# Kernel tuning notes

Measured on AMD Instinct MI355X. Metric: run time of the kernel, lower is better.

The kernel has to match this reference:

```python
import jax, jax.numpy as jnp
import numpy as np

H = 256   # hidden_dim
S = 16    # d_state
B = 2
N = 8192
LN_EPS = 1e-5


def setup_inputs() -> dict:
    key = jax.random.key(0)
    ks = jax.random.split(key, 12)
    std = 1.0 / np.sqrt(H)
    inp = {
        'x': jax.random.normal(ks[0], (B, N, H), dtype=jnp.float32),
        'in_w': jax.random.normal(ks[1], (2 * H, H), dtype=jnp.float32) * std,
        'in_b': jax.random.normal(ks[2], (2 * H,), dtype=jnp.float32) * std,
        'xp_w': jax.random.normal(ks[3], (2 * S + 1, H), dtype=jnp.float32) * std,
        'xp_b': jax.random.normal(ks[4], (2 * S + 1,), dtype=jnp.float32) * std,
        'dt_w': jax.random.normal(ks[5], (H, 1), dtype=jnp.float32),
        'dt_b': jax.random.normal(ks[6], (H,), dtype=jnp.float32),
        'A_log': jnp.log(jnp.broadcast_to(jnp.arange(1, S + 1, dtype=jnp.float32), (H, S))),
        'D': jnp.ones((H,), dtype=jnp.float32),
        'out_w': jax.random.normal(ks[7], (H, H), dtype=jnp.float32) * std,
        'out_b': jax.random.normal(ks[8], (H,), dtype=jnp.float32) * std,
        'ln_g': jnp.ones((H,), dtype=jnp.float32),
        'ln_b': jnp.zeros((H,), dtype=jnp.float32),
    }
    return inp


def reference(x, in_w, in_b, xp_w, xp_b, dt_w, dt_b, A_log, D, out_w, out_b, ln_g, ln_b):
    # x: (B, N, H). Dropout is identity in eval mode.
    residual = x
    xz = jnp.einsum('bnh,kh->bnk', x, in_w) + in_b            # (B,N,2H)
    x_inner, z = xz[..., :H], xz[..., H:]
    x_dbl = jnp.einsum('bnh,kh->bnk', x_inner, xp_w) + xp_b   # (B,N,2S+1)
    dt_raw = x_dbl[..., :1]
    B_raw = x_dbl[..., 1:S + 1]                               # (B,N,S)
    C_raw = x_dbl[..., S + 1:]                                # (B,N,S)
    dt = jax.nn.softplus(dt_raw * dt_w[:, 0] + dt_b)          # (B,N,H)
    # NOTE: the original computes dA = exp(dt * A) but never uses it; A_log
    # does not affect the output, so we skip materializing dA.
    dB = dt[..., None] * B_raw[:, :, None, :]                 # (B,N,H,S)
    h = jnp.cumsum(x_inner[..., None] * dB, axis=1)           # (B,N,H,S)
    y = jnp.einsum('bnhs,bns->bnh', h, C_raw) + D * x_inner   # (B,N,H)
    y = y * jax.nn.silu(z)
    out = jnp.einsum('bnh,kh->bnk', y, out_w) + out_b
    r = out + residual
    mu = jnp.mean(r, axis=-1, keepdims=True)
    var = jnp.mean((r - mu) ** 2, axis=-1, keepdims=True)
    return ln_g * (r - mu) * jax.lax.rsqrt(var + LN_EPS) + ln_b
```

## Files before the change

kernel.cpp:

```cpp
#include <hip/hip_runtime.h>
#include <hip/hip_bf16.h>


#define HD 256
#define SD 16
#define NSEQ 8192
#define NBATCH 2
#define BN (NBATCH * NSEQ)
#define CHUNK 32
#define NCHUNK (NSEQ / CHUNK)
#define NGRP 16
#define GSZ (NCHUNK / NGRP)
#define LN_EPS 1e-5f

#define NX  (BN * HD)
#define NIW (2 * HD * HD)
#define NXP (48 * HD)
#define NOW (HD * HD)

typedef __hip_bfloat16 bf16;
typedef __attribute__((ext_vector_type(8))) short bf16x8;
typedef __attribute__((ext_vector_type(4))) short short4v;
typedef __attribute__((ext_vector_type(4))) float f32x4;

__device__ __forceinline__ float b2f(bf16 v) { return __bfloat162float(v); }
__device__ __forceinline__ short f2bs(float f) {
  union { bf16 b; short s; } u;
  u.b = __float2bfloat16(f);
  return u.s;
}
__device__ __forceinline__ bf16x8 cvt_frag(const float* p) {
  bf16x8 r;
#pragma unroll
  for (int j = 0; j < 8; ++j) r[j] = f2bs(p[j]);
  return r;
}
__device__ __forceinline__ float softplus_f(float a) {
  return (a > 20.f) ? a : __logf(1.f + __expf(a));
}

__global__ __launch_bounds__(256) void k0_convert(
    const float* __restrict__ x, const float* __restrict__ in_w,
    const float* __restrict__ xp_w, const float* __restrict__ out_w,
    bf16* __restrict__ xb, bf16* __restrict__ wbin,
    bf16* __restrict__ wbxp, bf16* __restrict__ wbout)
{
  const int base = (blockIdx.x * 256 + threadIdx.x) * 4;
  if (base < NX) {
    f32x4 v = *(const f32x4*)(x + base);
    *(short4v*)((short*)xb + base) =
        short4v{f2bs(v[0]), f2bs(v[1]), f2bs(v[2]), f2bs(v[3])};
  } else if (base < NX + NIW) {
    const int off = base - NX;
    f32x4 v = *(const f32x4*)(in_w + off);
    *(short4v*)((short*)wbin + off) =
        short4v{f2bs(v[0]), f2bs(v[1]), f2bs(v[2]), f2bs(v[3])};
  } else if (base < NX + NIW + NXP) {
    const int off = base - NX - NIW;
    short4v s;
    if (off < 33 * HD) {
      f32x4 v = *(const f32x4*)(xp_w + off);
      s = short4v{f2bs(v[0]), f2bs(v[1]), f2bs(v[2]), f2bs(v[3])};
    } else {
      s = short4v{0, 0, 0, 0};
    }
    *(short4v*)((short*)wbxp + off) = s;
  } else if (base < NX + NIW + NXP + NOW) {
    const int off = base - NX - NIW - NXP;
    f32x4 v = *(const f32x4*)(out_w + off);
    *(short4v*)((short*)wbout + off) =
        short4v{f2bs(v[0]), f2bs(v[1]), f2bs(v[2]), f2bs(v[3])};
  }
}

__global__ __launch_bounds__(256) void k1_gemm(
    const bf16* __restrict__ xb, const bf16* __restrict__ wbin,
    const float* __restrict__ in_b, bf16* __restrict__ xib,
    bf16* __restrict__ zb)
{
  __shared__ __align__(16) char smem[128 * 264 * 2];
  bf16* Bt = (bf16*)smem;
  float* Ct = (float*)smem;

  const int tid = threadIdx.x;
  const int rt = blockIdx.x >> 2, ct = blockIdx.x & 3;
  const int R0 = rt * 128, C0 = ct * 128;
  const int wave = tid >> 6, lane = tid & 63, q = lane >> 4, l16 = lane & 15;

#pragma unroll
  for (int it = 0; it < 16; ++it) {
    const int f = tid + it * 256;
    const int row = f >> 5, g = f & 31;
    bf16x8 v = *(const bf16x8*)(wbin + (size_t)(C0 + row) * HD + g * 8);
    *(bf16x8*)(Bt + row * 264 + g * 8) = v;
  }
  __syncthreads();

  const int rowHalf = (wave & 1) * 64;
  const int colHalf = (wave >> 1) * 64;
  f32x4 acc[4][4] = {};
  const bf16* ap = xb + (size_t)(R0 + rowHalf + l16) * HD + q * 8;
#pragma unroll
  for (int k = 0; k < HD; k += 32) {
    bf16x8 a[4], b[4];
#pragma unroll
    for (int i = 0; i < 4; ++i)
      a[i] = *(const bf16x8*)(ap + (size_t)i * 16 * HD + k);
#pragma unroll
    for (int j = 0; j < 4; ++j)
      b[j] = *(const bf16x8*)(Bt + (colHalf + j * 16 + l16) * 264 + k + q * 8);
#pragma unroll
    for (int i = 0; i < 4; ++i)
#pragma unroll
      for (int j = 0; j < 4; ++j)
        acc[i][j] = __builtin_amdgcn_mfma_f32_16x16x32_bf16(a[i], b[j], acc[i][j], 0, 0, 0);
  }
  __syncthreads();

#pragma unroll
  for (int j = 0; j < 4; ++j) {
    const int col = colHalf + j * 16 + l16;
    const float bias = in_b[C0 + col];
#pragma unroll
    for (int i = 0; i < 4; ++i)
#pragma unroll
      for (int r = 0; r < 4; ++r)
        Ct[(rowHalf + i * 16 + q * 4 + r) * 132 + col] = acc[i][j][r] + bias;
  }
  __syncthreads();

  bf16* dst = (C0 < HD) ? xib : zb;
  const int Cd = (C0 < HD) ? C0 : (C0 - HD);
#pragma unroll
  for (int it = 0; it < 8; ++it) {
    const int f = tid + it * 256;
    const int row = f >> 4, g = f & 15;
    bf16x8 v = cvt_frag(Ct + row * 132 + g * 8);
    *(bf16x8*)(dst + (size_t)(R0 + row) * HD + Cd + g * 8) = v;
  }
}

__global__ __launch_bounds__(256) void k2_xp_sum(
    const bf16* __restrict__ xib, const bf16* __restrict__ wbxp,
    const float* __restrict__ xp_b, const float* __restrict__ dt_w,
    const float* __restrict__ dt_b, float* __restrict__ dbc,
    float* __restrict__ Mc)
{
  __shared__ bf16 xt[32 * 264];
  __shared__ bf16 wp[48 * 264];
  __shared__ float sdbc[32][33];
  const int tid = threadIdx.x;
  const int R0 = blockIdx.x * CHUNK;
  const int wave = tid >> 6, lane = tid & 63, q = lane >> 4, l16 = lane & 15;

#pragma unroll
  for (int it = 0; it < 4; ++it) {
    const int f = tid + it * 256, row = f >> 5, g = f & 31;
    *(bf16x8*)(xt + row * 264 + g * 8) =
        *(const bf16x8*)(xib + (size_t)(R0 + row) * HD + g * 8);
  }
#pragma unroll
  for (int it = 0; it < 6; ++it) {
    const int f = tid + it * 256, row = f >> 5, g = f & 31;
    *(bf16x8*)(wp + row * 264 + g * 8) =
        *(const bf16x8*)(wbxp + (size_t)row * HD + g * 8);
  }
  __syncthreads();

  if (wave < 2) {
    f32x4 pacc[3] = {};
#pragma unroll
    for (int k = 0; k < HD; k += 32) {
      bf16x8 af = *(const bf16x8*)(xt + (wave * 16 + l16) * 264 + k + q * 8);
#pragma unroll
      for (int t = 0; t < 3; ++t) {
        bf16x8 bfr = *(const bf16x8*)(wp + (t * 16 + l16) * 264 + k + q * 8);
        pacc[t] = __builtin_amdgcn_mfma_f32_16x16x32_bf16(af, bfr, pacc[t], 0, 0, 0);
      }
    }
#pragma unroll
    for (int t = 0; t < 3; ++t) {
      const int col = t * 16 + l16;
      if (col < 33) {
        const float bias = xp_b[col];
#pragma unroll
        for (int r = 0; r < 4; ++r)
          sdbc[wave * 16 + q * 4 + r][col] = pacc[t][r] + bias;
      }
    }
  }
  __syncthreads();

  {
    const float* sflat = &sdbc[0][0];
    for (int idx = tid; idx < CHUNK * 33; idx += 256)
      dbc[(size_t)R0 * 33 + idx] = sflat[idx];
  }
  {
    const int h = tid;
    const float dtw = dt_w[h], dtb = dt_b[h];
    float st[SD] = {};
#pragma unroll
    for (int n = 0; n < CHUNK; ++n) {
      const float xv = b2f(xt[n * 264 + h]);
      const float dt = softplus_f(sdbc[n][0] * dtw + dtb);
      const float u = xv * dt;
#pragma unroll
      for (int s = 0; s < SD; ++s) st[s] += u * sdbc[n][1 + s];
    }
    const int b = R0 >> 13, c = (R0 & (NSEQ - 1)) >> 5;
    float* mp = Mc + ((size_t)(b * NCHUNK + c)) * 4096 + h;
#pragma unroll
    for (int s = 0; s < SD; ++s) mp[s * HD] = st[s];
  }
}

__global__ __launch_bounds__(256) void k4a_prefix_local(
    float* __restrict__ Mc, float* __restrict__ Gs)
{
  const int tid = blockIdx.x * 256 + threadIdx.x;
  const int b = tid >> 16;
  const int g = (tid >> 12) & (NGRP - 1);
  const int hs = tid & 4095;
  float run = 0.f;
#pragma unroll
  for (int i = 0; i < GSZ; ++i) {
    const size_t idx = ((size_t)(b * NCHUNK + g * GSZ + i)) * 4096 + hs;
    const float v = Mc[idx];
    Mc[idx] = run;
    run += v;
  }
  Gs[((size_t)(b * NGRP + g)) * 4096 + hs] = run;
}

__global__ __launch_bounds__(256) void k4b_prefix_groups(float* __restrict__ Gs)
{
  const int tid = blockIdx.x * 256 + threadIdx.x;
  const int b = tid >> 12;
  const int hs = tid & 4095;
  float run = 0.f;
#pragma unroll
  for (int g = 0; g < NGRP; ++g) {
    const size_t idx = ((size_t)(b * NGRP + g)) * 4096 + hs;
    const float v = Gs[idx];
    Gs[idx] = run;
    run += v;
  }
}

__global__ __launch_bounds__(512) void k56_scan_out_ln(
    const bf16* __restrict__ xib, const bf16* __restrict__ zb,
    const float* __restrict__ dbc, const float* __restrict__ dt_w,
    const float* __restrict__ dt_b, const float* __restrict__ Dv,
    const float* __restrict__ Mc, const float* __restrict__ Gs,
    const bf16* __restrict__ wbout, const float* __restrict__ out_b,
    const float* __restrict__ x, const float* __restrict__ ln_g,
    const float* __restrict__ ln_b, float* __restrict__ out)
{
  __shared__ float sdbc[CHUNK][33];
  __shared__ float yt[32][260];
  __shared__ float pt[32][260];
  const int tid = threadIdx.x;
  const int wave = tid >> 6, lane = tid & 63, q = lane >> 4, l16 = lane & 15;
  const int R0 = blockIdx.x * CHUNK;
  const int b = R0 >> 13;
  const int cchunk = (R0 & (NSEQ - 1)) >> 5;

  for (int idx = tid; idx < CHUNK * 33; idx += 512) {
    const int n = idx / 33, j = idx - n * 33;
    sdbc[n][j] = dbc[(size_t)(R0 + n) * 33 + j];
  }
  __syncthreads();

  {
    const int h = tid & 255;
    const int sh = tid >> 8;
    const float dtw = dt_w[h], dtb = dt_b[h];
    const float dv = Dv[h];
    float st[8];
    const float* mp = Mc + ((size_t)(b * NCHUNK + cchunk)) * 4096 + sh * 8 * HD + h;
    const float* gp = Gs + ((size_t)(b * NGRP + cchunk / GSZ)) * 4096 + sh * 8 * HD + h;
#pragma unroll
    for (int s = 0; s < 8; ++s) st[s] = mp[s * HD] + gp[s * HD];
    float (*dst)[260] = (sh == 0) ? yt : pt;
    for (int n = 0; n < CHUNK; ++n) {
      const float xv = b2f(xib[(size_t)(R0 + n) * HD + h]);
      const float dt = softplus_f(sdbc[n][0] * dtw + dtb);
      const float u = xv * dt;
      float y = (sh == 0) ? dv * xv : 0.f;
#pragma unroll
      for (int s = 0; s < 8; ++s) {
        st[s] += u * sdbc[n][1 + sh * 8 + s];
        y += st[s] * sdbc[n][17 + sh * 8 + s];
      }
      dst[n][h] = y;
    }
  }
  __syncthreads();

  {
    const int h = tid & 255;
    const int r2 = tid >> 8;
#pragma unroll
    for (int j = 0; j < 16; ++j) {
      const int row = r2 * 16 + j;
      const float zv = b2f(zb[(size_t)(R0 + row) * HD + h]);
      const float sig = 1.f / (1.f + __expf(-zv));
      yt[row][h] = (yt[row][h] + pt[row][h]) * zv * sig;
    }
  }
  __syncthreads();

  const int cw = wave * 32;
  f32x4 acc[2][2] = {};
#pragma unroll
  for (int k = 0; k < HD; k += 32) {
    bf16x8 a0 = cvt_frag(&yt[l16][k + q * 8]);
    bf16x8 a1 = cvt_frag(&yt[16 + l16][k + q * 8]);
#pragma unroll
    for (int t = 0; t < 2; ++t) {
      bf16x8 bfr = *(const bf16x8*)(wbout + (size_t)(cw + t * 16 + l16) * HD + k + q * 8);
      acc[0][t] = __builtin_amdgcn_mfma_f32_16x16x32_bf16(a0, bfr, acc[0][t], 0, 0, 0);
      acc[1][t] = __builtin_amdgcn_mfma_f32_16x16x32_bf16(a1, bfr, acc[1][t], 0, 0, 0);
    }
  }
  __syncthreads();

#pragma unroll
  for (int t = 0; t < 2; ++t) {
    const int col = cw + t * 16 + l16;
    const float bias = out_b[col];
#pragma unroll
    for (int i = 0; i < 2; ++i)
#pragma unroll
      for (int r = 0; r < 4; ++r) {
        const int row = i * 16 + q * 4 + r;
        pt[row][col] = acc[i][t][r] + bias + x[(size_t)(R0 + row) * HD + col];
      }
  }
  __syncthreads();

#pragma unroll
  for (int rr = 0; rr < 4; ++rr) {
    const int row = wave * 4 + rr;
    float p = 0.f;
#pragma unroll
    for (int j = 0; j < 4; ++j) p += pt[row][lane + 64 * j];
#pragma unroll
    for (int off = 32; off > 0; off >>= 1) p += __shfl_xor(p, off);
    const float mu = p * (1.f / 256.f);
    float v2 = 0.f;
#pragma unroll
    for (int j = 0; j < 4; ++j) {
      const float d = pt[row][lane + 64 * j] - mu;
      v2 += d * d;
    }
#pragma unroll
    for (int off = 32; off > 0; off >>= 1) v2 += __shfl_xor(v2, off);
    const float rstd = rsqrtf(v2 * (1.f / 256.f) + LN_EPS);
    const size_t base = (size_t)(R0 + row) * HD;
#pragma unroll
    for (int j = 0; j < 4; ++j) {
      const int cc = lane + 64 * j;
      out[base + cc] = ln_g[cc] * (pt[row][cc] - mu) * rstd + ln_b[cc];
    }
  }
}

extern "C" void kernel_launch(void* const* d_in, const int* in_sizes, int n_in,
                              void* d_out, int out_size, void* d_ws, size_t ws_size,
                              hipStream_t stream)
{
  const float* x     = (const float*)d_in[0];
  const float* in_w  = (const float*)d_in[1];
  const float* in_b  = (const float*)d_in[2];
  const float* xp_w  = (const float*)d_in[3];
  const float* xp_b  = (const float*)d_in[4];
  const float* dt_w  = (const float*)d_in[5];
  const float* dt_b  = (const float*)d_in[6];
  const float* Dv    = (const float*)d_in[8];
  const float* out_w = (const float*)d_in[9];
  const float* out_b = (const float*)d_in[10];
  const float* ln_g  = (const float*)d_in[11];
  const float* ln_b  = (const float*)d_in[12];

  char* ws = (char*)d_ws;
  bf16*  xib   = (bf16*)(ws);
  bf16*  zb    = (bf16*)(ws +  8388608);
  bf16*  xb    = (bf16*)(ws + 16777216);
  float* dbc   = (float*)(ws + 25165824);
  float* Mc    = (float*)(ws + 27328512);
  float* Gs    = (float*)(ws + 35717120);
  bf16*  wbin  = (bf16*)(ws + 36241408);
  bf16*  wbxp  = (bf16*)(ws + 36503552);
  bf16*  wbout = (bf16*)(ws + 36528128);
  float* out   = (float*)d_out;

  hipLaunchKernelGGL(k0_convert, dim3((NX + NIW + NXP + NOW) / 1024), dim3(256),
                     0, stream, x, in_w, xp_w, out_w, xb, wbin, wbxp, wbout);
  hipLaunchKernelGGL(k1_gemm, dim3(512), dim3(256), 0, stream,
                     xb, wbin, in_b, xib, zb);
  hipLaunchKernelGGL(k2_xp_sum, dim3(BN / CHUNK), dim3(256), 0, stream,
                     xib, wbxp, xp_b, dt_w, dt_b, dbc, Mc);
  hipLaunchKernelGGL(k4a_prefix_local, dim3(NBATCH * NGRP * 4096 / 256),
                     dim3(256), 0, stream, Mc, Gs);
  hipLaunchKernelGGL(k4b_prefix_groups, dim3(NBATCH * 4096 / 256), dim3(256),
                     0, stream, Gs);
  hipLaunchKernelGGL(k56_scan_out_ln, dim3(BN / CHUNK), dim3(512), 0, stream,
                     xib, zb, dbc, dt_w, dt_b, Dv, Mc, Gs,
                     wbout, out_b, x, ln_g, ln_b, out);
}
```

Measured before the change: 150.3 us.

## Reformulate chunked SSM scan as MFMA matmuls with precomputed masked C·B tile

The per-chunk state sums and the intra-chunk scan become bf16 MFMA products. The chunk-end state is B^T·U. The output is a causal-masked (C·B^T)·U plus C·H_prev, with the masked 32x32 T matrix computed in the xp kernel and passed through global memory. This replaces the serial per-thread scalar recurrence over 16 states and 32 timesteps with matrix-core work, and shrinks the output kernel to 256 threads with reused shared memory. In exchange, the scan state, B, C and u are rounded to bf16, which lowers accuracy, and an extra global buffer write and read is added.

```diff
diff --git a/kernel.cpp b/kernel.cpp
--- a/kernel.cpp
+++ b/kernel.cpp
@@ -12,6 +12,8 @@
 #define NGRP 16
 #define GSZ (NCHUNK / NGRP)
 #define LN_EPS 1e-5f
+#define UST 40
+#define YST 257
 
 #define NX  (BN * HD)
 #define NIW (2 * HD * HD)
@@ -22,12 +24,18 @@
 typedef __attribute__((ext_vector_type(8))) short bf16x8;
 typedef __attribute__((ext_vector_type(4))) short short4v;
 typedef __attribute__((ext_vector_type(4))) float f32x4;
+typedef __attribute__((ext_vector_type(4))) unsigned int uint4v;
+typedef __attribute__((ext_vector_type(2))) unsigned int uint2v;
 
 __device__ __forceinline__ float b2f(bf16 v) { return __bfloat162float(v); }
 __device__ __forceinline__ short f2bs(float f) {
   union { bf16 b; short s; } u;
   u.b = __float2bfloat16(f);
   return u.s;
+}
+__device__ __forceinline__ unsigned int pack2(float a, float b) {
+  return (unsigned int)(unsigned short)f2bs(a) |
+         ((unsigned int)(unsigned short)f2bs(b) << 16);
 }
 __device__ __forceinline__ bf16x8 cvt_frag(const float* p) {
   bf16x8 r;
@@ -140,18 +148,21 @@
   }
 }
 
-__global__ __launch_bounds__(256) void k2_xp_sum(
+__global__ __launch_bounds__(256) void kS_xp_sum(
     const bf16* __restrict__ xib, const bf16* __restrict__ wbxp,
     const float* __restrict__ xp_b, const float* __restrict__ dt_w,
     const float* __restrict__ dt_b, float* __restrict__ dbc,
-    float* __restrict__ Mc)
-{
-  __shared__ bf16 xt[32 * 264];
-  __shared__ bf16 wp[48 * 264];
-  __shared__ float sdbc[32][33];
+    bf16* __restrict__ Tg, float* __restrict__ Mc)
+{
+  __shared__ __align__(16) bf16 xt[32 * 264];
+  __shared__ __align__(16) bf16 wp[48 * 264];
+  __shared__ __align__(16) float sdbc[32][33];
+  __shared__ __align__(16) bf16 sBt[16 * UST];
+  __shared__ __align__(16) bf16 Ut[256 * UST];
   const int tid = threadIdx.x;
-  const int R0 = blockIdx.x * CHUNK;
   const int wave = tid >> 6, lane = tid & 63, q = lane >> 4, l16 = lane & 15;
+  const int cix = blockIdx.x;
+  const int R0 = cix * CHUNK;
 
 #pragma unroll
   for (int it = 0; it < 4; ++it) {
@@ -184,8 +195,13 @@
       if (col < 33) {
         const float bias = xp_b[col];
 #pragma unroll
-        for (int r = 0; r < 4; ++r)
-          sdbc[wave * 16 + q * 4 + r][col] = pacc[t][r] + bias;
+        for (int r = 0; r < 4; ++r) {
+          const int row = wave * 16 + q * 4 + r;
+          const float v = pacc[t][r] + bias;
+          sdbc[row][col] = v;
+          if (col >= 1 && col < 17)
+            *((short*)sBt + (col - 1) * UST + row) = f2bs(v);
+        }
       }
     }
   }
@@ -199,19 +215,57 @@
   {
     const int h = tid;
     const float dtw = dt_w[h], dtb = dt_b[h];
-    float st[SD] = {};
-#pragma unroll
-    for (int n = 0; n < CHUNK; ++n) {
-      const float xv = b2f(xt[n * 264 + h]);
-      const float dt = softplus_f(sdbc[n][0] * dtw + dtb);
-      const float u = xv * dt;
-#pragma unroll
-      for (int s = 0; s < SD; ++s) st[s] += u * sdbc[n][1 + s];
-    }
-    const int b = R0 >> 13, c = (R0 & (NSEQ - 1)) >> 5;
-    float* mp = Mc + ((size_t)(b * NCHUNK + c)) * 4096 + h;
-#pragma unroll
-    for (int s = 0; s < SD; ++s) mp[s * HD] = st[s];
+    unsigned int up[16];
+#pragma unroll
+    for (int n2 = 0; n2 < 16; ++n2) {
+      const int n = 2 * n2;
+      const float xv0 = b2f(xt[n * 264 + h]);
+      const float xv1 = b2f(xt[(n + 1) * 264 + h]);
+      const float u0 = xv0 * softplus_f(sdbc[n][0] * dtw + dtb);
+      const float u1 = xv1 * softplus_f(sdbc[n + 1][0] * dtw + dtb);
+      up[n2] = pack2(u0, u1);
+    }
+    uint4v* dst = (uint4v*)(Ut + h * UST);
+#pragma unroll
+    for (int j = 0; j < 4; ++j)
+      dst[j] = uint4v{up[4 * j], up[4 * j + 1], up[4 * j + 2], up[4 * j + 3]};
+  }
+  {
+    const int n = tid >> 3;
+    const int m0 = (tid & 7) * 4;
+    float cn[SD];
+#pragma unroll
+    for (int s = 0; s < SD; ++s) cn[s] = sdbc[n][17 + s];
+    short4v tv;
+#pragma unroll
+    for (int mm = 0; mm < 4; ++mm) {
+      const int m = m0 + mm;
+      float t = 0.f;
+#pragma unroll
+      for (int s = 0; s < SD; ++s) t += cn[s] * sdbc[m][1 + s];
+      tv[mm] = (m <= n) ? f2bs(t) : (short)0;
+    }
+    *(short4v*)((short*)Tg + (size_t)cix * 1024 + n * 32 + m0) = tv;
+  }
+  __syncthreads();
+
+  {
+    bf16x8 af = *(const bf16x8*)(sBt + l16 * UST + q * 8);
+    f32x4 macc[4] = {};
+#pragma unroll
+    for (int c4 = 0; c4 < 4; ++c4) {
+      const int ct = wave * 4 + c4;
+      bf16x8 bu = *(const bf16x8*)(Ut + (ct * 16 + l16) * UST + q * 8);
+      macc[c4] = __builtin_amdgcn_mfma_f32_16x16x32_bf16(af, bu, macc[c4], 0, 0, 0);
+    }
+    float* mbase = Mc + (size_t)cix * 4096;
+#pragma unroll
+    for (int c4 = 0; c4 < 4; ++c4) {
+      const int h = (wave * 4 + c4) * 16 + l16;
+#pragma unroll
+      for (int r = 0; r < 4; ++r)
+        mbase[(q * 4 + r) * HD + h] = macc[c4][r];
+    }
   }
 }
 
@@ -248,111 +302,169 @@
   }
 }
 
-__global__ __launch_bounds__(512) void k56_scan_out_ln(
+__global__ __launch_bounds__(256) void k56_scan_out_ln(
     const bf16* __restrict__ xib, const bf16* __restrict__ zb,
-    const float* __restrict__ dbc, const float* __restrict__ dt_w,
-    const float* __restrict__ dt_b, const float* __restrict__ Dv,
-    const float* __restrict__ Mc, const float* __restrict__ Gs,
-    const bf16* __restrict__ wbout, const float* __restrict__ out_b,
-    const float* __restrict__ x, const float* __restrict__ ln_g,
-    const float* __restrict__ ln_b, float* __restrict__ out)
-{
-  __shared__ float sdbc[CHUNK][33];
-  __shared__ float yt[32][260];
-  __shared__ float pt[32][260];
+    const float* __restrict__ dbc, const bf16* __restrict__ Tg,
+    const float* __restrict__ dt_w, const float* __restrict__ dt_b,
+    const float* __restrict__ Dv, const float* __restrict__ Mc,
+    const float* __restrict__ Gs, const bf16* __restrict__ wbout,
+    const float* __restrict__ out_b, const float* __restrict__ x,
+    const float* __restrict__ ln_g, const float* __restrict__ ln_b,
+    float* __restrict__ out)
+{
+  __shared__ __align__(16) char un[2 * 32 * YST * 4];
+  bf16* Ut  = (bf16*)un;
+  bf16* Hst = (bf16*)(un + 20480);
+  bf16* Ctl = (bf16*)(un + 40960);
+  bf16* Tt  = (bf16*)(un + 43520);
+  float* yt = (float*)un;
+  float* pt = (float*)(un + 32 * YST * 4);
+  __shared__ float sdt[32];
+
   const int tid = threadIdx.x;
   const int wave = tid >> 6, lane = tid & 63, q = lane >> 4, l16 = lane & 15;
-  const int R0 = blockIdx.x * CHUNK;
-  const int b = R0 >> 13;
-  const int cchunk = (R0 & (NSEQ - 1)) >> 5;
-
-  for (int idx = tid; idx < CHUNK * 33; idx += 512) {
-    const int n = idx / 33, j = idx - n * 33;
-    sdbc[n][j] = dbc[(size_t)(R0 + n) * 33 + j];
-  }
-  __syncthreads();
-
-  {
-    const int h = tid & 255;
-    const int sh = tid >> 8;
+  const int cix = blockIdx.x;
+  const int R0 = cix * CHUNK;
+  const int b = cix >> 8;
+  const int cchunk = cix & 255;
+
+  *(short4v*)((short*)Tt + tid * 4) =
+      *(const short4v*)((const short*)Tg + (size_t)cix * 1024 + tid * 4);
+  if (tid < 32) sdt[tid] = dbc[(size_t)(R0 + tid) * 33];
+  {
+    const int n = tid >> 3, k0 = (tid & 7) * 4;
+    float v[4];
+#pragma unroll
+    for (int j = 0; j < 4; ++j) {
+      const int k = k0 + j;
+      v[j] = (k < SD) ? dbc[(size_t)(R0 + n) * 33 + 17 + k] : 0.f;
+    }
+    *(uint2v*)((short*)Ctl + n * UST + k0) = uint2v{pack2(v[0], v[1]), pack2(v[2], v[3])};
+  }
+  {
+    const int h = tid;
+    const float* mp = Mc + (size_t)cix * 4096 + h;
+    const float* gp = Gs + ((size_t)(b * NGRP + cchunk / GSZ)) * 4096 + h;
+    unsigned int hp[8];
+#pragma unroll
+    for (int s2 = 0; s2 < 8; ++s2) {
+      const int s = 2 * s2;
+      const float v0 = mp[s * HD] + gp[s * HD];
+      const float v1 = mp[(s + 1) * HD] + gp[(s + 1) * HD];
+      hp[s2] = pack2(v0, v1);
+    }
+    uint4v* hd = (uint4v*)(Hst + h * UST);
+    hd[0] = uint4v{hp[0], hp[1], hp[2], hp[3]};
+    hd[1] = uint4v{hp[4], hp[5], hp[6], hp[7]};
+    hd[2] = uint4v{0, 0, 0, 0};
+    hd[3] = uint4v{0, 0, 0, 0};
+  }
+  __syncthreads();
+
+  {
+    const int h = tid;
     const float dtw = dt_w[h], dtb = dt_b[h];
-    const float dv = Dv[h];
-    float st[8];
-    const float* mp = Mc + ((size_t)(b * NCHUNK + cchunk)) * 4096 + sh * 8 * HD + h;
-    const float* gp = Gs + ((size_t)(b * NGRP + cchunk / GSZ)) * 4096 + sh * 8 * HD + h;
-#pragma unroll
-    for (int s = 0; s < 8; ++s) st[s] = mp[s * HD] + gp[s * HD];
-    float (*dst)[260] = (sh == 0) ? yt : pt;
+    unsigned int up[16];
+#pragma unroll
+    for (int n2 = 0; n2 < 16; ++n2) {
+      const int n = 2 * n2;
+      const float xv0 = b2f(xib[(size_t)(R0 + n) * HD + h]);
+      const float xv1 = b2f(xib[(size_t)(R0 + n + 1) * HD + h]);
+      const float u0 = xv0 * softplus_f(sdt[n] * dtw + dtb);
+      const float u1 = xv1 * softplus_f(sdt[n + 1] * dtw + dtb);
+      up[n2] = pack2(u0, u1);
+    }
+    uint4v* dst = (uint4v*)(Ut + h * UST);
+#pragma unroll
+    for (int j = 0; j < 4; ++j)
+      dst[j] = uint4v{up[4 * j], up[4 * j + 1], up[4 * j + 2], up[4 * j + 3]};
+  }
+  __syncthreads();
+
+  f32x4 acc[2][4] = {};
+  {
+    bf16x8 aT0 = *(const bf16x8*)(Tt + l16 * 32 + q * 8);
+    bf16x8 aT1 = *(const bf16x8*)(Tt + (16 + l16) * 32 + q * 8);
+    bf16x8 aC0 = *(const bf16x8*)(Ctl + l16 * UST + q * 8);
+    bf16x8 aC1 = *(const bf16x8*)(Ctl + (16 + l16) * UST + q * 8);
+#pragma unroll
+    for (int c4 = 0; c4 < 4; ++c4) {
+      const int ct = wave * 4 + c4;
+      bf16x8 bu = *(const bf16x8*)(Ut + (ct * 16 + l16) * UST + q * 8);
+      bf16x8 bh = *(const bf16x8*)(Hst + (ct * 16 + l16) * UST + q * 8);
+      acc[0][c4] = __builtin_amdgcn_mfma_f32_16x16x32_bf16(aT0, bu, acc[0][c4], 0, 0, 0);
+      acc[0][c4] = __builtin_amdgcn_mfma_f32_16x16x32_bf16(aC0, bh, acc[0][c4], 0, 0, 0);
+      acc[1][c4] = __builtin_amdgcn_mfma_f32_16x16x32_bf16(aT1, bu, acc[1][c4], 0, 0, 0);
+      acc[1][c4] = __builtin_amdgcn_mfma_f32_16x16x32_bf16(aC1, bh, acc[1][c4], 0, 0, 0);
+    }
+  }
+  __syncthreads();
+
+#pragma unroll
+  for (int c4 = 0; c4 < 4; ++c4) {
+    const int h = (wave * 4 + c4) * 16 + l16;
+#pragma unroll
+    for (int rt = 0; rt < 2; ++rt)
+#pragma unroll
+      for (int r = 0; r < 4; ++r)
+        yt[(rt * 16 + q * 4 + r) * YST + h] = acc[rt][c4][r];
+  }
+  __syncthreads();
+
+  {
+    const int h = tid;
+    const float dh = Dv[h];
+#pragma unroll
     for (int n = 0; n < CHUNK; ++n) {
-      const float xv = b2f(xib[(size_t)(R0 + n) * HD + h]);
-      const float dt = softplus_f(sdbc[n][0] * dtw + dtb);
-      const float u = xv * dt;
-      float y = (sh == 0) ? dv * xv : 0.f;
-#pragma unroll
-      for (int s = 0; s < 8; ++s) {
-        st[s] += u * sdbc[n][1 + sh * 8 + s];
-        y += st[s] * sdbc[n][17 + sh * 8 + s];
-      }
-      dst[n][h] = y;
-    }
-  }
-  __syncthreads();
-
-  {
-    const int h = tid & 255;
-    const int r2 = tid >> 8;
-#pragma unroll
-    for (int j = 0; j < 16; ++j) {
-      const int row = r2 * 16 + j;
-      const float zv = b2f(zb[(size_t)(R0 + row) * HD + h]);
+      const size_t row = (size_t)(R0 + n) * HD + h;
+      const float yv = yt[n * YST + h] + dh * b2f(xib[row]);
+      const float zv = b2f(zb[row]);
       const float sig = 1.f / (1.f + __expf(-zv));
-      yt[row][h] = (yt[row][h] + pt[row][h]) * zv * sig;
-    }
-  }
-  __syncthreads();
-
-  const int cw = wave * 32;
-  f32x4 acc[2][2] = {};
+      yt[n * YST + h] = yv * zv * sig;
+    }
+  }
+  __syncthreads();
+
+  const int cw = wave * 64;
+  f32x4 oacc[2][4] = {};
 #pragma unroll
   for (int k = 0; k < HD; k += 32) {
-    bf16x8 a0 = cvt_frag(&yt[l16][k + q * 8]);
-    bf16x8 a1 = cvt_frag(&yt[16 + l16][k + q * 8]);
-#pragma unroll
-    for (int t = 0; t < 2; ++t) {
+    bf16x8 a0 = cvt_frag(&yt[l16 * YST + k + q * 8]);
+    bf16x8 a1 = cvt_frag(&yt[(16 + l16) * YST + k + q * 8]);
+#pragma unroll
+    for (int t = 0; t < 4; ++t) {
       bf16x8 bfr = *(const bf16x8*)(wbout + (size_t)(cw + t * 16 + l16) * HD + k + q * 8);
-      acc[0][t] = __builtin_amdgcn_mfma_f32_16x16x32_bf16(a0, bfr, acc[0][t], 0, 0, 0);
-      acc[1][t] = __builtin_amdgcn_mfma_f32_16x16x32_bf16(a1, bfr, acc[1][t], 0, 0, 0);
-    }
-  }
-  __syncthreads();
-
-#pragma unroll
-  for (int t = 0; t < 2; ++t) {
+      oacc[0][t] = __builtin_amdgcn_mfma_f32_16x16x32_bf16(a0, bfr, oacc[0][t], 0, 0, 0);
+      oacc[1][t] = __builtin_amdgcn_mfma_f32_16x16x32_bf16(a1, bfr, oacc[1][t], 0, 0, 0);
+    }
+  }
+#pragma unroll
+  for (int t = 0; t < 4; ++t) {
     const int col = cw + t * 16 + l16;
     const float bias = out_b[col];
 #pragma unroll
-    for (int i = 0; i < 2; ++i)
+    for (int rt = 0; rt < 2; ++rt)
 #pragma unroll
       for (int r = 0; r < 4; ++r) {
-        const int row = i * 16 + q * 4 + r;
-        pt[row][col] = acc[i][t][r] + bias + x[(size_t)(R0 + row) * HD + col];
+        const int row = rt * 16 + q * 4 + r;
+        pt[row * YST + col] = oacc[rt][t][r] + bias + x[(size_t)(R0 + row) * HD + col];
       }
   }
   __syncthreads();
 
 #pragma unroll
-  for (int rr = 0; rr < 4; ++rr) {
-    const int row = wave * 4 + rr;
+  for (int rr = 0; rr < 8; ++rr) {
+    const int row = wave * 8 + rr;
     float p = 0.f;
 #pragma unroll
-    for (int j = 0; j < 4; ++j) p += pt[row][lane + 64 * j];
+    for (int j = 0; j < 4; ++j) p += pt[row * YST + lane + 64 * j];
 #pragma unroll
     for (int off = 32; off > 0; off >>= 1) p += __shfl_xor(p, off);
     const float mu = p * (1.f / 256.f);
     float v2 = 0.f;
 #pragma unroll
     for (int j = 0; j < 4; ++j) {
-      const float d = pt[row][lane + 64 * j] - mu;
+      const float d = pt[row * YST + lane + 64 * j] - mu;
       v2 += d * d;
     }
 #pragma unroll
@@ -362,7 +474,7 @@
 #pragma unroll
     for (int j = 0; j < 4; ++j) {
       const int cc = lane + 64 * j;
-      out[base + cc] = ln_g[cc] * (pt[row][cc] - mu) * rstd + ln_b[cc];
+      out[base + cc] = ln_g[cc] * (pt[row * YST + cc] - mu) * rstd + ln_b[cc];
     }
   }
 }
@@ -394,19 +506,20 @@
   bf16*  wbin  = (bf16*)(ws + 36241408);
   bf16*  wbxp  = (bf16*)(ws + 36503552);
   bf16*  wbout = (bf16*)(ws + 36528128);
+  bf16*  Tg    = (bf16*)(ws + 36659200);
   float* out   = (float*)d_out;
 
   hipLaunchKernelGGL(k0_convert, dim3((NX + NIW + NXP + NOW) / 1024), dim3(256),
                      0, stream, x, in_w, xp_w, out_w, xb, wbin, wbxp, wbout);
   hipLaunchKernelGGL(k1_gemm, dim3(512), dim3(256), 0, stream,
                      xb, wbin, in_b, xib, zb);
-  hipLaunchKernelGGL(k2_xp_sum, dim3(BN / CHUNK), dim3(256), 0, stream,
-                     xib, wbxp, xp_b, dt_w, dt_b, dbc, Mc);
+  hipLaunchKernelGGL(kS_xp_sum, dim3(BN / CHUNK), dim3(256), 0, stream,
+                     xib, wbxp, xp_b, dt_w, dt_b, dbc, Tg, Mc);
   hipLaunchKernelGGL(k4a_prefix_local, dim3(NBATCH * NGRP * 4096 / 256),
                      dim3(256), 0, stream, Mc, Gs);
   hipLaunchKernelGGL(k4b_prefix_groups, dim3(NBATCH * 4096 / 256), dim3(256),
                      0, stream, Gs);
-  hipLaunchKernelGGL(k56_scan_out_ln, dim3(BN / CHUNK), dim3(512), 0, stream,
-                     xib, zb, dbc, dt_w, dt_b, Dv, Mc, Gs,
+  hipLaunchKernelGGL(k56_scan_out_ln, dim3(BN / CHUNK), dim3(256), 0, stream,
+                     xib, zb, dbc, Tg, dt_w, dt_b, Dv, Mc, Gs,
                      wbout, out_b, x, ln_g, ln_b, out);
 }
```

Result: faster. 144.0 us (-4.2%).
